# Kernel optimization log

Hardware: AMD Instinct MI355X
Metric: run time of the kernel (lower is better)

Reference implementation:

```python
import jax, jax.numpy as jnp
import numpy as np
import math

DILATION_RATES = (1, 2, 4, 8)


def setup_inputs() -> dict:
    key = jax.random.key(0)
    B, S, D = 2, 2048, 512
    R = len(DILATION_RATES)
    ks = jax.random.split(key, 8)
    s = 0.02  # init scale
    x = jax.random.normal(ks[0], (B, S, D), dtype=jnp.float32)
    Wq = jax.random.normal(ks[1], (D, D), dtype=jnp.float32) * s
    Wk = jax.random.normal(ks[2], (D, D), dtype=jnp.float32) * s
    Wv = jax.random.normal(ks[3], (D, D), dtype=jnp.float32) * s
    Wr = jax.random.normal(ks[4], (R, D, D), dtype=jnp.float32) * s  # per-rate projections
    Wo = jax.random.normal(ks[5], (R * D, D), dtype=jnp.float32) * s
    bq = jnp.zeros((D,), jnp.float32)
    bk = jnp.zeros((D,), jnp.float32)
    bv = jnp.zeros((D,), jnp.float32)
    br = jnp.zeros((R, D), jnp.float32)
    bo = jnp.zeros((D,), jnp.float32)
    return {"x": x, "Wq": Wq, "bq": bq, "Wk": Wk, "bk": bk, "Wv": Wv, "bv": bv,
            "Wr": Wr, "br": br, "Wo": Wo, "bo": bo}


def reference(x, Wq, bq, Wk, bk, Wv, bv, Wr, br, Wo, bo):
    B, S, D = x.shape
    Q = x @ Wq + bq
    K = x @ Wk + bk
    V = x @ Wv + bv
    # Dense scores are identical across rates in the original (recomputed each loop);
    # compute once for the same math.
    scores = jnp.einsum('bid,bjd->bij', Q, K) / math.sqrt(D)  # [B,S,S]
    idx = jnp.arange(S)
    outs, attns = [], []
    for r, rate in enumerate(DILATION_RATES):
        # mask[i, j] = 1 iff (j % rate == 0) and (j <= i)
        mask = (idx[None, :] % rate == 0) & (idx[None, :] <= idx[:, None])  # [S,S]
        sc = jnp.where(mask[None, :, :], scores, jnp.float32(-1e9))
        attn = jax.nn.softmax(sc, axis=-1)  # dropout is identity at eval
        attns.append(attn)
        ctx = jnp.einsum('bij,bjd->bid', attn, V)
        outs.append(ctx @ Wr[r] + br[r])
    combined = jnp.concatenate(outs, axis=-1)  # [B,S,4D]
    output = combined @ Wo + bo  # [B,S,D]
    avg_attention = jnp.mean(jnp.stack(attns, axis=0), axis=0)  # [B,S,S]
    return output, avg_attention
```

## Files before the change

kernel.cpp:

```cpp
#include <hip/hip_runtime.h>
#include <hip/hip_bf16.h>
#include <math.h>

#define B_ 2
#define S_ 2048
#define D_ 512
#define R_ 4
#define KP 3840

typedef __attribute__((ext_vector_type(8))) __bf16 bf16x8;
typedef __attribute__((ext_vector_type(4))) float f32x4;

enum { M_QKV = 0, M_SCORES = 1, M_WEFFT = 2, M_W2T = 3, M_PF = 4 };

__device__ __forceinline__ void g2l16(const void* gp, void* lp) {
    __builtin_amdgcn_global_load_lds(
        (const __attribute__((address_space(1))) unsigned int*)(unsigned long long)gp,
        (__attribute__((address_space(3))) unsigned int*)(unsigned int)(unsigned long long)lp,
        16, 0, 0);
}

template<int MODE, int TBM, int TBN>
__global__ __launch_bounds__(256) void mfma_nt(
    const short* __restrict__ A, const short* __restrict__ B,
    const float* __restrict__ bias, void* __restrict__ Cv,
    int lda, int ldb, int ldc, int K,
    long strA, long strB, long strC, long strBias, float scale)
{
    constexpr int WM = TBM / 2, WN = TBN / 2;
    constexpr int FM = WM / 16, FN = WN / 16;

    __shared__ __bf16 sAt[TBM * 128];
    __shared__ __bf16 sBt[TBN * 128];

    const int tid  = threadIdx.x;
    const int lane = tid & 63, wid = tid >> 6;
    const int ln15 = lane & 15, quad = lane >> 4;
    const int wy = wid & 1, wx = wid >> 1;

    const int by   = (MODE == M_PF) ? (gridDim.y - 1 - blockIdx.y) : blockIdx.y;
    const int col0 = blockIdx.x * TBN;
    const int row0 = by * TBM;
    const int z    = blockIdx.z;

    if constexpr (MODE == M_SCORES) {
        if (col0 > row0 + TBM - 1) return;
    }

    const short* Ab = A + (size_t)z * strA;
    const short* Bb = B + (size_t)z * strB;
    const float* biasb = bias + (size_t)z * strBias;

    int rate = 1, seg = 0;
    if constexpr (MODE == M_W2T) {
        int rIdx;
        if      (col0 >= 3584) { rate = 8; seg = 3584; rIdx = 3; }
        else if (col0 >= 3072) { rate = 4; seg = 3072; rIdx = 2; }
        else if (col0 >= 2048) { rate = 2; seg = 2048; rIdx = 1; }
        else                   { rate = 1; seg = 0;    rIdx = 0; }
        Ab += (size_t)rIdx * D_ * D_;
    }

    f32x4 acc[FM][FN];
    #pragma unroll
    for (int u = 0; u < FM; ++u)
        #pragma unroll
        for (int v = 0; v < FN; ++v)
            acc[u][v] = (f32x4){0.f, 0.f, 0.f, 0.f};

    for (int k0 = 0; k0 < K; k0 += 128) {
        if constexpr (MODE == M_PF) {
            int kr, ks;
            if      (k0 >= 3584) { kr = 8; ks = 3584; }
            else if (k0 >= 3072) { kr = 4; ks = 3072; }
            else if (k0 >= 2048) { kr = 2; ks = 2048; }
            else                 { kr = 1; ks = 0;    }
            if ((k0 - ks) * kr > row0 + TBM - 1) continue;
        }

        #pragma unroll
        for (int t = 0; t < TBM * 16; t += 256) {
            int idx = t + tid;
            int r = idx >> 4, clog = (idx & 15) ^ (r & 7);
            const short* g = Ab + (size_t)(row0 + r) * lda + k0 + clog * 8;
            g2l16(g, (char*)sAt + (t + wid * 64) * 16);
        }
        #pragma unroll
        for (int t = 0; t < TBN * 16; t += 256) {
            int idx = t + tid;
            int r = idx >> 4, clog = (idx & 15) ^ (r & 7);
            int grow;
            if constexpr (MODE == M_W2T) grow = (col0 + r - seg) * rate;
            else                         grow = col0 + r;
            const short* g = Bb + (size_t)grow * ldb + k0 + clog * 8;
            g2l16(g, (char*)sBt + (t + wid * 64) * 16);
        }
        __syncthreads();

        #pragma unroll
        for (int kk = 0; kk < 128; kk += 32) {
            bf16x8 af[FM], bfr[FN];
            #pragma unroll
            for (int u = 0; u < FM; ++u) {
                int ra = wy * WM + u * 16 + ln15;
                int ch = (kk >> 3) + quad;
                af[u] = *(const bf16x8*)&sAt[ra * 128 + (ch ^ (ra & 7)) * 8];
            }
            #pragma unroll
            for (int v = 0; v < FN; ++v) {
                int rb = wx * WN + v * 16 + ln15;
                int ch = (kk >> 3) + quad;
                bfr[v] = *(const bf16x8*)&sBt[rb * 128 + (ch ^ (rb & 7)) * 8];
            }
            #pragma unroll
            for (int u = 0; u < FM; ++u)
                #pragma unroll
                for (int v = 0; v < FN; ++v)
                    acc[u][v] = __builtin_amdgcn_mfma_f32_16x16x32_bf16(
                        af[u], bfr[v], acc[u][v], 0, 0, 0);
        }
        __syncthreads();
    }

    constexpr bool OUTBF = (MODE == M_QKV || MODE == M_WEFFT || MODE == M_W2T);
    #pragma unroll
    for (int u = 0; u < FM; ++u) {
        int rg = row0 + wy * WM + u * 16 + quad * 4;
        #pragma unroll
        for (int v = 0; v < FN; ++v) {
            int cg = col0 + wx * WN + v * 16 + ln15;
            float bv = 0.f;
            if constexpr (MODE == M_QKV || MODE == M_PF) bv = biasb[cg];
            #pragma unroll
            for (int rr = 0; rr < 4; ++rr) {
                float val = acc[u][v][rr];
                if constexpr (MODE == M_SCORES) val *= scale;
                val += bv;
                if constexpr (OUTBF)
                    ((__hip_bfloat16*)Cv)[(size_t)z * strC + (size_t)(rg + rr) * ldc + cg] =
                        __float2bfloat16(val);
                else
                    ((float*)Cv)[(size_t)z * strC + (size_t)(rg + rr) * ldc + cg] = val;
            }
        }
    }
}

__global__ __launch_bounds__(256) void prep_cvt(const float* __restrict__ x,
                                                const float* __restrict__ Wr,
                                                __hip_bfloat16* __restrict__ xb,
                                                __hip_bfloat16* __restrict__ Wrb)
{
    const size_t NX = (size_t)B_ * S_ * D_;
    size_t i = ((size_t)blockIdx.x * 256 + threadIdx.x) * 4;
    const float* in; __hip_bfloat16* out; size_t off;
    if (i < NX) { in = x; out = xb; off = i; }
    else        { in = Wr; out = Wrb; off = i - NX; }
    float4 v = *(const float4*)(in + off);
    out[off + 0] = __float2bfloat16(v.x);
    out[off + 1] = __float2bfloat16(v.y);
    out[off + 2] = __float2bfloat16(v.z);
    out[off + 3] = __float2bfloat16(v.w);
}

__global__ __launch_bounds__(256) void prep_transpose(const float* __restrict__ Wq,
                                                      const float* __restrict__ Wk,
                                                      const float* __restrict__ Wv,
                                                      const float* __restrict__ Wo,
                                                      __hip_bfloat16* __restrict__ WqT,
                                                      __hip_bfloat16* __restrict__ WoT)
{
    __shared__ float t[32][33];
    int y = blockIdx.y;
    const float* in; __hip_bfloat16* out; int Rr, r0;
    if (y < 48) {
        int w = y >> 4;
        in = (w == 0) ? Wq : (w == 1) ? Wk : Wv;
        out = WqT + (size_t)w * 512 * 512;
        Rr = 512; r0 = (y & 15) * 32;
    } else {
        in = Wo; out = WoT; Rr = 2048; r0 = (y - 48) * 32;
    }
    int c0 = blockIdx.x * 32;
    int tx = threadIdx.x & 31, ty = threadIdx.x >> 5;
    #pragma unroll
    for (int dy = 0; dy < 32; dy += 8)
        t[ty + dy][tx] = in[(size_t)(r0 + ty + dy) * 512 + c0 + tx];
    __syncthreads();
    #pragma unroll
    for (int dy = 0; dy < 32; dy += 8)
        out[(size_t)(c0 + ty + dy) * Rr + r0 + tx] = __float2bfloat16(t[tx][ty + dy]);
}

__global__ __launch_bounds__(512) void prep_small(const float* __restrict__ bq,
                                                  const float* __restrict__ bk,
                                                  const float* __restrict__ bv,
                                                  const float* __restrict__ bo,
                                                  float* __restrict__ biasqkv,
                                                  float* __restrict__ beff)
{
    int t = threadIdx.x;
    biasqkv[t]        = bq[t];
    biasqkv[512 + t]  = bk[t];
    biasqkv[1024 + t] = bv[t];
    beff[t]           = bo[t];
}

__global__ __launch_bounds__(512) void beff_acc(const float* __restrict__ br,
                                                const float* __restrict__ Wo,
                                                float* __restrict__ beff)
{
    int n  = threadIdx.x;
    int m0 = blockIdx.x * 128;
    float acc = 0.f;
    #pragma unroll 4
    for (int m = m0; m < m0 + 128; ++m)
        acc += br[m] * Wo[(size_t)m * D_ + n];
    atomicAdd(&beff[n], acc);
}

__global__ __launch_bounds__(256) void softmax_p(const float* __restrict__ scores,
                                                 float* __restrict__ avg_out,
                                                 __hip_bfloat16* __restrict__ P)
{
    __shared__ float s_p[S_];
    __shared__ float red[4];
    __shared__ float bs[8];

    int i   = blockIdx.x;
    int b   = blockIdx.y;
    int tid = threadIdx.x;
    int wv  = tid >> 6;
    int ln  = tid & 63;

    const float* srow = scores + ((size_t)b * S_ + i) * S_;
    __bf16* prow = (__bf16*)(P + ((size_t)b * S_ + i) * KP);

    const int cnt1 = i + 1;
    const int n4   = cnt1 >> 2;

    float m = -INFINITY;
    for (int t = tid; t < n4; t += 256) {
        float4 v = ((const float4*)srow)[t];
        ((float4*)s_p)[t] = v;
        m = fmaxf(m, fmaxf(fmaxf(v.x, v.y), fmaxf(v.z, v.w)));
    }
    for (int j = (n4 << 2) + tid; j < cnt1; j += 256) {
        float v = srow[j]; s_p[j] = v; m = fmaxf(m, v);
    }
    #pragma unroll
    for (int o = 32; o > 0; o >>= 1) m = fmaxf(m, __shfl_xor(m, o, 64));
    if (ln == 0) red[wv] = m;
    if (tid < 8) bs[tid] = 0.f;
    __syncthreads();
    m = fmaxf(fmaxf(red[0], red[1]), fmaxf(red[2], red[3]));

    float a0 = 0.f, a1 = 0.f, a2 = 0.f, a3 = 0.f;
    for (int t = tid; t < n4; t += 256) {
        float4 v = ((float4*)s_p)[t];
        v.x = __expf(v.x - m); v.y = __expf(v.y - m);
        v.z = __expf(v.z - m); v.w = __expf(v.w - m);
        ((float4*)s_p)[t] = v;
        a0 += v.x; a1 += v.y; a2 += v.z; a3 += v.w;
    }
    for (int j = (n4 << 2) + tid; j < cnt1; j += 256) {
        float e = __expf(s_p[j] - m); s_p[j] = e;
        atomicAdd(&bs[j & 7], e);
    }
    float o0 = __shfl_xor(a0, 1, 64), o1 = __shfl_xor(a1, 1, 64);
    float o2 = __shfl_xor(a2, 1, 64), o3 = __shfl_xor(a3, 1, 64);
    float b8[8];
    if ((ln & 1) == 0) {
        b8[0]=a0; b8[1]=a1; b8[2]=a2; b8[3]=a3; b8[4]=o0; b8[5]=o1; b8[6]=o2; b8[7]=o3;
    } else {
        b8[0]=o0; b8[1]=o1; b8[2]=o2; b8[3]=o3; b8[4]=a0; b8[5]=a1; b8[6]=a2; b8[7]=a3;
    }
    #pragma unroll
    for (int st = 2; st < 64; st <<= 1)
        #pragma unroll
        for (int k = 0; k < 8; ++k) b8[k] += __shfl_xor(b8[k], st, 64);
    if (ln == 0) {
        #pragma unroll
        for (int k = 0; k < 8; ++k) atomicAdd(&bs[k], b8[k]);
    }
    __syncthreads();

    float S1 = bs[0]+bs[1]+bs[2]+bs[3]+bs[4]+bs[5]+bs[6]+bs[7];
    float S2 = bs[0]+bs[2]+bs[4]+bs[6];
    float S4 = bs[0]+bs[4];
    float S8 = bs[0];
    float i1 = 1.f/S1, i2 = 1.f/S2, i4 = 1.f/S4, i8 = 1.f/S8;
    float c0 = 0.25f*(i1+i2+i4+i8), c1 = 0.25f*i1, c2 = 0.25f*(i1+i2);
    float c4 = 0.25f*(i1+i2+i4);
    float cA[4] = {c0, c1, c2, c1};
    float cB[4] = {c4, c1, c2, c1};

    float* arow = avg_out + ((size_t)b * S_ + i) * S_;
    for (int t = tid; t < S_ / 4; t += 256) {
        int j = t << 2;
        float4 e = ((float4*)s_p)[t];
        const float* cc = (t & 1) ? cB : cA;
        float4 o;
        o.x = (j     < cnt1) ? e.x * cc[0] : 0.f;
        o.y = (j + 1 < cnt1) ? e.y * cc[1] : 0.f;
        o.z = (j + 2 < cnt1) ? e.z * cc[2] : 0.f;
        o.w = (j + 3 < cnt1) ? e.w * cc[3] : 0.f;
        ((float4*)arow)[t] = o;
    }

    const float invSr[4] = {i1, i2, i4, i8};
    const int   segoff[4] = {0, 2048, 3072, 3584};
    const int   imax = i | 63;
    #pragma unroll
    for (int ri = 0; ri < 4; ++ri) {
        int seg    = segoff[ri];
        int segLen = S_ >> ri;
        int cnt    = (i >> ri) + 1;
        int tlim   = min(segLen, ((imax >> ri) & ~127) + 128);
        float invS = invSr[ri];
        int nch = tlim >> 3;
        for (int t8 = tid; t8 < nch; t8 += 256) {
            int t0 = t8 << 3;
            bf16x8 w;
            #pragma unroll
            for (int k = 0; k < 8; ++k) {
                int t = t0 + k;
                float p = (t < cnt) ? s_p[t << ri] * invS : 0.f;
                w[k] = (__bf16)p;
            }
            *((bf16x8*)(prow + seg) + t8) = w;
        }
    }
}

extern "C" void kernel_launch(void* const* d_in, const int* in_sizes, int n_in,
                              void* d_out, int out_size, void* d_ws, size_t ws_size,
                              hipStream_t stream)
{
    const float* x  = (const float*)d_in[0];
    const float* Wq = (const float*)d_in[1];
    const float* bq = (const float*)d_in[2];
    const float* Wk = (const float*)d_in[3];
    const float* bk = (const float*)d_in[4];
    const float* Wv = (const float*)d_in[5];
    const float* bv = (const float*)d_in[6];
    const float* Wr = (const float*)d_in[7];
    const float* br = (const float*)d_in[8];
    const float* Wo = (const float*)d_in[9];
    const float* bo = (const float*)d_in[10];

    float* out    = (float*)d_out;
    float* scores = out + (size_t)B_ * S_ * D_;

    char* wsb = (char*)d_ws;
    short* xb  = (short*)(wsb);
    short* Qb  = (short*)(wsb + (4u << 20));
    short* Kb  = (short*)(wsb + (8u << 20));
    short* Vb  = (short*)(wsb + (12u << 20));
    short* P   = (short*)(wsb + (16u << 20));
    short* W2T = (short*)(wsb + (16u << 20) + 31457280u);
    float* beff    = (float*)(wsb + (16u << 20) + 31457280u + 7864320u);
    float* biasqkv = beff + 512;
    short* WqT   = P;
    short* Wrb   = (short*)((char*)P + 1572864);
    short* WoT   = (short*)((char*)P + 3670016);
    short* WeffT = (short*)((char*)P + 5767168);

    const float scale = (float)(1.0 / sqrt((double)D_));

    prep_small<<<1, 512, 0, stream>>>(bq, bk, bv, bo, biasqkv, beff);
    beff_acc<<<16, 512, 0, stream>>>(br, Wo, beff);
    prep_cvt<<<dim3(3072), 256, 0, stream>>>(x, Wr, (__hip_bfloat16*)xb,
                                             (__hip_bfloat16*)Wrb);
    prep_transpose<<<dim3(16, 112), 256, 0, stream>>>(
        Wq, Wk, Wv, Wo, (__hip_bfloat16*)WqT, (__hip_bfloat16*)WoT);

    mfma_nt<M_QKV, 64, 128><<<dim3(4, 64, 3), 256, 0, stream>>>(
        xb, WqT, biasqkv, Qb, 512, 512, 512, 512,
        0, 512L * 512, (long)B_ * S_ * D_, 512, 0.f);

    mfma_nt<M_SCORES, 64, 128><<<dim3(16, 32, 2), 256, 0, stream>>>(
        Qb, Kb, beff, scores, 512, 512, 2048, 512,
        (long)S_ * D_, (long)S_ * D_, (long)S_ * S_, 0, scale);

    mfma_nt<M_WEFFT, 64, 64><<<dim3(8, 8, 4), 256, 0, stream>>>(
        WoT, Wrb, beff, WeffT, 2048, 512, 512, 512,
        512, (long)D_ * D_, (long)D_ * D_, 0, 0.f);

    mfma_nt<M_W2T, 64, 128><<<dim3(30, 8, 2), 256, 0, stream>>>(
        WeffT, Vb, beff, W2T, 512, 512, 3840, 512,
        0, (long)S_ * D_, 512L * KP, 0, 0.f);

    softmax_p<<<dim3(S_, B_), 256, 0, stream>>>(scores, scores, (__hip_bfloat16*)P);

    mfma_nt<M_PF, 64, 64><<<dim3(8, 32, 2), 256, 0, stream>>>(
        P, W2T, beff, out, 3840, 3840, 512, 3840,
        (long)S_ * KP, 512L * KP, (long)S_ * D_, 0, 0.f);
}
```

Before: 207.4 us.

## Merge launches into fused multi-role kernels and store scores as bf16

Collapses the four prep kernels into one multi-role kernel, with bias partial sums replacing atomics. It also fuses the QKV and Weff GEMMs with the bias reduction, and the scores and W2T GEMMs, into shared launches. Scores now go as bf16 into the P buffer instead of fp32 into the output region, which cuts launch count and the fp32 scores traffic in softmax. Reading scores back as bf16 lowers softmax input precision and adds a reuse hazard on the P buffer.

```diff
diff --git a/kernel.cpp b/kernel.cpp
--- a/kernel.cpp
+++ b/kernel.cpp
@@ -21,27 +21,25 @@
 }
 
 template<int MODE, int TBM, int TBN>
-__global__ __launch_bounds__(256) void mfma_nt(
+__device__ __forceinline__ void mfma_body(
+    int bx, int by, int bz,
     const short* __restrict__ A, const short* __restrict__ B,
     const float* __restrict__ bias, void* __restrict__ Cv,
     int lda, int ldb, int ldc, int K,
-    long strA, long strB, long strC, long strBias, float scale)
+    long strA, long strB, long strC, long strBias, float scale,
+    __bf16* sAt, __bf16* sBt)
 {
     constexpr int WM = TBM / 2, WN = TBN / 2;
     constexpr int FM = WM / 16, FN = WN / 16;
-
-    __shared__ __bf16 sAt[TBM * 128];
-    __shared__ __bf16 sBt[TBN * 128];
 
     const int tid  = threadIdx.x;
     const int lane = tid & 63, wid = tid >> 6;
     const int ln15 = lane & 15, quad = lane >> 4;
     const int wy = wid & 1, wx = wid >> 1;
 
-    const int by   = (MODE == M_PF) ? (gridDim.y - 1 - blockIdx.y) : blockIdx.y;
-    const int col0 = blockIdx.x * TBN;
+    const int col0 = bx * TBN;
     const int row0 = by * TBM;
-    const int z    = blockIdx.z;
+    const int z    = bz;
 
     if constexpr (MODE == M_SCORES) {
         if (col0 > row0 + TBM - 1) return;
@@ -122,7 +120,7 @@
         __syncthreads();
     }
 
-    constexpr bool OUTBF = (MODE == M_QKV || MODE == M_WEFFT || MODE == M_W2T);
+    constexpr bool OUTBF = (MODE != M_PF);
     #pragma unroll
     for (int u = 0; u < FM; ++u) {
         int rg = row0 + wy * WM + u * 16 + quad * 4;
@@ -146,81 +144,132 @@
     }
 }
 
-__global__ __launch_bounds__(256) void prep_cvt(const float* __restrict__ x,
-                                                const float* __restrict__ Wr,
-                                                __hip_bfloat16* __restrict__ xb,
-                                                __hip_bfloat16* __restrict__ Wrb)
-{
-    const size_t NX = (size_t)B_ * S_ * D_;
-    size_t i = ((size_t)blockIdx.x * 256 + threadIdx.x) * 4;
-    const float* in; __hip_bfloat16* out; size_t off;
-    if (i < NX) { in = x; out = xb; off = i; }
-    else        { in = Wr; out = Wrb; off = i - NX; }
-    float4 v = *(const float4*)(in + off);
-    out[off + 0] = __float2bfloat16(v.x);
-    out[off + 1] = __float2bfloat16(v.y);
-    out[off + 2] = __float2bfloat16(v.z);
-    out[off + 3] = __float2bfloat16(v.w);
-}
-
-__global__ __launch_bounds__(256) void prep_transpose(const float* __restrict__ Wq,
-                                                      const float* __restrict__ Wk,
-                                                      const float* __restrict__ Wv,
-                                                      const float* __restrict__ Wo,
-                                                      __hip_bfloat16* __restrict__ WqT,
-                                                      __hip_bfloat16* __restrict__ WoT)
-{
-    __shared__ float t[32][33];
-    int y = blockIdx.y;
-    const float* in; __hip_bfloat16* out; int Rr, r0;
-    if (y < 48) {
-        int w = y >> 4;
-        in = (w == 0) ? Wq : (w == 1) ? Wk : Wv;
-        out = WqT + (size_t)w * 512 * 512;
-        Rr = 512; r0 = (y & 15) * 32;
+__global__ __launch_bounds__(256) void prep_all(
+    const float* __restrict__ x,  const float* __restrict__ Wr,
+    const float* __restrict__ Wq, const float* __restrict__ Wk,
+    const float* __restrict__ Wv, const float* __restrict__ Wo,
+    const float* __restrict__ bq, const float* __restrict__ bk,
+    const float* __restrict__ bv, const float* __restrict__ br,
+    __hip_bfloat16* __restrict__ xb,  __hip_bfloat16* __restrict__ Wrb,
+    __hip_bfloat16* __restrict__ WqT, __hip_bfloat16* __restrict__ WoT,
+    float* __restrict__ biasqkv, float* __restrict__ beff_part)
+{
+    __shared__ float tsh[32][33];
+    const int f = blockIdx.x, tid = threadIdx.x;
+
+    if (f < 3072) {
+        const float* in; __hip_bfloat16* out; size_t off;
+        if (f < 2048) { in = x;  out = xb;  off = ((size_t)f * 256 + tid) * 4; }
+        else          { in = Wr; out = Wrb; off = ((size_t)(f - 2048) * 256 + tid) * 4; }
+        float4 v = *(const float4*)(in + off);
+        out[off + 0] = __float2bfloat16(v.x);
+        out[off + 1] = __float2bfloat16(v.y);
+        out[off + 2] = __float2bfloat16(v.z);
+        out[off + 3] = __float2bfloat16(v.w);
+    } else if (f < 4864) {
+        int g = f - 3072;
+        int cx = g & 15, y = g >> 4;
+        const float* in; __hip_bfloat16* out; int Rr, r0;
+        if (y < 48) {
+            int w = y >> 4;
+            in = (w == 0) ? Wq : (w == 1) ? Wk : Wv;
+            out = WqT + (size_t)w * 512 * 512;
+            Rr = 512; r0 = (y & 15) * 32;
+        } else {
+            in = Wo; out = WoT; Rr = 2048; r0 = (y - 48) * 32;
+        }
+        int c0 = cx * 32;
+        int tx = tid & 31, ty = tid >> 5;
+        #pragma unroll
+        for (int dy = 0; dy < 32; dy += 8)
+            tsh[ty + dy][tx] = in[(size_t)(r0 + ty + dy) * 512 + c0 + tx];
+        __syncthreads();
+        #pragma unroll
+        for (int dy = 0; dy < 32; dy += 8)
+            out[(size_t)(c0 + ty + dy) * Rr + r0 + tx] = __float2bfloat16(tsh[tx][ty + dy]);
+    } else if (f < 4880) {
+        int j = f - 4864, m0 = j * 128;
+        float a0 = 0.f, a1 = 0.f;
+        for (int m = m0; m < m0 + 128; ++m) {
+            float b = br[m];
+            a0 += b * Wo[(size_t)m * D_ + tid];
+            a1 += b * Wo[(size_t)m * D_ + tid + 256];
+        }
+        beff_part[j * 512 + tid]       = a0;
+        beff_part[j * 512 + tid + 256] = a1;
     } else {
-        in = Wo; out = WoT; Rr = 2048; r0 = (y - 48) * 32;
-    }
-    int c0 = blockIdx.x * 32;
-    int tx = threadIdx.x & 31, ty = threadIdx.x >> 5;
-    #pragma unroll
-    for (int dy = 0; dy < 32; dy += 8)
-        t[ty + dy][tx] = in[(size_t)(r0 + ty + dy) * 512 + c0 + tx];
-    __syncthreads();
-    #pragma unroll
-    for (int dy = 0; dy < 32; dy += 8)
-        out[(size_t)(c0 + ty + dy) * Rr + r0 + tx] = __float2bfloat16(t[tx][ty + dy]);
-}
-
-__global__ __launch_bounds__(512) void prep_small(const float* __restrict__ bq,
-                                                  const float* __restrict__ bk,
-                                                  const float* __restrict__ bv,
-                                                  const float* __restrict__ bo,
-                                                  float* __restrict__ biasqkv,
-                                                  float* __restrict__ beff)
-{
-    int t = threadIdx.x;
-    biasqkv[t]        = bq[t];
-    biasqkv[512 + t]  = bk[t];
-    biasqkv[1024 + t] = bv[t];
-    beff[t]           = bo[t];
-}
-
-__global__ __launch_bounds__(512) void beff_acc(const float* __restrict__ br,
-                                                const float* __restrict__ Wo,
-                                                float* __restrict__ beff)
-{
-    int n  = threadIdx.x;
-    int m0 = blockIdx.x * 128;
-    float acc = 0.f;
-    #pragma unroll 4
-    for (int m = m0; m < m0 + 128; ++m)
-        acc += br[m] * Wo[(size_t)m * D_ + n];
-    atomicAdd(&beff[n], acc);
-}
-
-__global__ __launch_bounds__(256) void softmax_p(const float* __restrict__ scores,
-                                                 float* __restrict__ avg_out,
+        for (int k = tid; k < 512; k += 256) {
+            biasqkv[k]        = bq[k];
+            biasqkv[512 + k]  = bk[k];
+            biasqkv[1024 + k] = bv[k];
+        }
+    }
+}
+
+__global__ __launch_bounds__(256) void k_qkv_wefft(
+    const short* __restrict__ xb, const short* __restrict__ WqT,
+    const float* __restrict__ biasqkv, short* __restrict__ Qb,
+    const short* __restrict__ WoT, const short* __restrict__ Wrb,
+    short* __restrict__ WeffT,
+    const float* __restrict__ beff_part, const float* __restrict__ bo,
+    float* __restrict__ beff)
+{
+    __shared__ __bf16 sA[64 * 128];
+    __shared__ __bf16 sB[128 * 128];
+    int f = blockIdx.x;
+    if (f < 768) {
+        mfma_body<M_QKV, 64, 128>(f & 3, (f >> 2) & 63, f >> 8,
+            xb, WqT, biasqkv, Qb, 512, 512, 512, 512,
+            0, 512L * 512, (long)B_ * S_ * D_, 512, 0.f, sA, sB);
+    } else if (f < 896) {
+        int g = f - 768;
+        mfma_body<M_WEFFT, 64, 128>(g & 3, (g >> 2) & 7, g >> 5,
+            WoT, Wrb, beff, WeffT, 2048, 512, 512, 512,
+            512, (long)D_ * D_, (long)D_ * D_, 0, 0.f, sA, sB);
+    } else {
+        int t = threadIdx.x;
+        for (int n = t; n < 512; n += 256) {
+            float a = bo[n];
+            #pragma unroll
+            for (int j = 0; j < 16; ++j) a += beff_part[j * 512 + n];
+            beff[n] = a;
+        }
+    }
+}
+
+__global__ __launch_bounds__(256) void k_scores_w2t(
+    const short* __restrict__ Qb, const short* __restrict__ Kb,
+    short* __restrict__ P, const short* __restrict__ WeffT,
+    const short* __restrict__ Vb, short* __restrict__ W2T,
+    const float* __restrict__ dummy, float scale)
+{
+    __shared__ __bf16 sA[64 * 128];
+    __shared__ __bf16 sB[128 * 128];
+    int f = blockIdx.x;
+    if (f < 1024) {
+        mfma_body<M_SCORES, 64, 128>(f & 15, (f >> 4) & 31, f >> 9,
+            Qb, Kb, dummy, P, 512, 512, KP, 512,
+            (long)S_ * D_, (long)S_ * D_, (long)S_ * KP, 0, scale, sA, sB);
+    } else {
+        int g = f - 1024;
+        mfma_body<M_W2T, 64, 128>(g % 30, (g / 30) & 7, g / 240,
+            WeffT, Vb, dummy, W2T, 512, 512, KP, 512,
+            0, (long)S_ * D_, 512L * KP, 0, 0.f, sA, sB);
+    }
+}
+
+__global__ __launch_bounds__(256) void k_pf(
+    const short* __restrict__ P, const short* __restrict__ W2T,
+    const float* __restrict__ beff, float* __restrict__ out)
+{
+    __shared__ __bf16 sA[64 * 128];
+    __shared__ __bf16 sB[64 * 128];
+    mfma_body<M_PF, 64, 64>(blockIdx.x, gridDim.y - 1 - blockIdx.y, blockIdx.z,
+        P, W2T, beff, out, KP, KP, 512, KP,
+        (long)S_ * KP, 512L * KP, (long)S_ * D_, 0, 0.f, sA, sB);
+}
+
+__global__ __launch_bounds__(256) void softmax_p(float* __restrict__ avg_out,
                                                  __hip_bfloat16* __restrict__ P)
 {
     __shared__ float s_p[S_];
@@ -233,20 +282,22 @@
     int wv  = tid >> 6;
     int ln  = tid & 63;
 
-    const float* srow = scores + ((size_t)b * S_ + i) * S_;
-    __bf16* prow = (__bf16*)(P + ((size_t)b * S_ + i) * KP);
+    __bf16* prow = (__bf16*)P + ((size_t)b * S_ + i) * KP;
 
     const int cnt1 = i + 1;
+    const int nchL = (cnt1 + 7) >> 3;
     const int n4   = cnt1 >> 2;
 
     float m = -INFINITY;
-    for (int t = tid; t < n4; t += 256) {
-        float4 v = ((const float4*)srow)[t];
-        ((float4*)s_p)[t] = v;
-        m = fmaxf(m, fmaxf(fmaxf(v.x, v.y), fmaxf(v.z, v.w)));
-    }
-    for (int j = (n4 << 2) + tid; j < cnt1; j += 256) {
-        float v = srow[j]; s_p[j] = v; m = fmaxf(m, v);
+    for (int t = tid; t < nchL; t += 256) {
+        bf16x8 v = ((const bf16x8*)prow)[t];
+        int base = t << 3;
+        #pragma unroll
+        for (int k = 0; k < 8; ++k) {
+            float xv = (base + k < cnt1) ? (float)v[k] : -INFINITY;
+            s_p[base + k] = xv;
+            m = fmaxf(m, xv);
+        }
     }
     #pragma unroll
     for (int o = 32; o > 0; o >>= 1) m = fmaxf(m, __shfl_xor(m, o, 64));
@@ -308,7 +359,7 @@
         ((float4*)arow)[t] = o;
     }
 
-    const float invSr[4] = {i1, i2, i4, i8};
+    const float invSr[4]  = {i1, i2, i4, i8};
     const int   segoff[4] = {0, 2048, 3072, 3584};
     const int   imax = i | 63;
     #pragma unroll
@@ -349,51 +400,37 @@
     const float* Wo = (const float*)d_in[9];
     const float* bo = (const float*)d_in[10];
 
-    float* out    = (float*)d_out;
-    float* scores = out + (size_t)B_ * S_ * D_;
+    float* out = (float*)d_out;
+    float* avg = out + (size_t)B_ * S_ * D_;
 
     char* wsb = (char*)d_ws;
     short* xb  = (short*)(wsb);
-    short* Qb  = (short*)(wsb + (4u << 20));
-    short* Kb  = (short*)(wsb + (8u << 20));
+    short* Qb  = (short*)(wsb + (4u  << 20));
     short* Vb  = (short*)(wsb + (12u << 20));
     short* P   = (short*)(wsb + (16u << 20));
     short* W2T = (short*)(wsb + (16u << 20) + 31457280u);
-    float* beff    = (float*)(wsb + (16u << 20) + 31457280u + 7864320u);
-    float* biasqkv = beff + 512;
-    short* WqT   = P;
-    short* Wrb   = (short*)((char*)P + 1572864);
-    short* WoT   = (short*)((char*)P + 3670016);
-    short* WeffT = (short*)((char*)P + 5767168);
+    short* WqT = W2T;
+    short* Wrb   = (short*)((char*)W2T + 7864320u);
+    short* WoT   = (short*)((char*)Wrb + 2097152u);
+    short* WeffT = (short*)((char*)WoT + 2097152u);
+    float* beff      = (float*)((char*)WeffT + 2097152u);
+    float* biasqkv   = beff + 512;
+    float* beff_part = biasqkv + 1536;
 
     const float scale = (float)(1.0 / sqrt((double)D_));
 
-    prep_small<<<1, 512, 0, stream>>>(bq, bk, bv, bo, biasqkv, beff);
-    beff_acc<<<16, 512, 0, stream>>>(br, Wo, beff);
-    prep_cvt<<<dim3(3072), 256, 0, stream>>>(x, Wr, (__hip_bfloat16*)xb,
-                                             (__hip_bfloat16*)Wrb);
-    prep_transpose<<<dim3(16, 112), 256, 0, stream>>>(
-        Wq, Wk, Wv, Wo, (__hip_bfloat16*)WqT, (__hip_bfloat16*)WoT);
-
-    mfma_nt<M_QKV, 64, 128><<<dim3(4, 64, 3), 256, 0, stream>>>(
-        xb, WqT, biasqkv, Qb, 512, 512, 512, 512,
-        0, 512L * 512, (long)B_ * S_ * D_, 512, 0.f);
-
-    mfma_nt<M_SCORES, 64, 128><<<dim3(16, 32, 2), 256, 0, stream>>>(
-        Qb, Kb, beff, scores, 512, 512, 2048, 512,
-        (long)S_ * D_, (long)S_ * D_, (long)S_ * S_, 0, scale);
-
-    mfma_nt<M_WEFFT, 64, 64><<<dim3(8, 8, 4), 256, 0, stream>>>(
-        WoT, Wrb, beff, WeffT, 2048, 512, 512, 512,
-        512, (long)D_ * D_, (long)D_ * D_, 0, 0.f);
-
-    mfma_nt<M_W2T, 64, 128><<<dim3(30, 8, 2), 256, 0, stream>>>(
-        WeffT, Vb, beff, W2T, 512, 512, 3840, 512,
-        0, (long)S_ * D_, 512L * KP, 0, 0.f);
-
-    softmax_p<<<dim3(S_, B_), 256, 0, stream>>>(scores, scores, (__hip_bfloat16*)P);
-
-    mfma_nt<M_PF, 64, 64><<<dim3(8, 32, 2), 256, 0, stream>>>(
-        P, W2T, beff, out, 3840, 3840, 512, 3840,
-        (long)S_ * KP, 512L * KP, (long)S_ * D_, 0, 0.f);
-}
+    prep_all<<<dim3(4881), 256, 0, stream>>>(
+        x, Wr, Wq, Wk, Wv, Wo, bq, bk, bv, br,
+        (__hip_bfloat16*)xb, (__hip_bfloat16*)Wrb,
+        (__hip_bfloat16*)WqT, (__hip_bfloat16*)WoT, biasqkv, beff_part);
+
+    k_qkv_wefft<<<dim3(897), 256, 0, stream>>>(
+        xb, WqT, biasqkv, Qb, WoT, Wrb, WeffT, beff_part, bo, beff);
+
+    k_scores_w2t<<<dim3(1504), 256, 0, stream>>>(
+        Qb, Qb + (size_t)B_ * S_ * D_, P, WeffT, Vb, W2T, beff, scale);
+
+    softmax_p<<<dim3(S_, B_), 256, 0, stream>>>(avg, (__hip_bfloat16*)P);
+
+    k_pf<<<dim3(8, 32, 2), 256, 0, stream>>>(P, W2T, beff, out);
+}
```

Result: slower. 212.6 us (+2.5%).
